# Performance work log

Hardware: AMD Instinct MI355X
Metric: run time of the kernel (lower is better)

## Reference

```python
import jax, jax.numpy as jnp
import numpy as np

B, L, V = 16, 2048, 64


def setup_inputs() -> dict:
    key = jax.random.key(0)
    k1, k2, k3, k4 = jax.random.split(key, 4)
    idx = jax.random.randint(k1, (B, L), 0, V)                      # tokens
    Wq_w = jax.random.normal(k2, (V, V), jnp.float32) * 0.02         # nn.Linear weight
    Wv_w = jax.random.normal(k3, (V, V), jnp.float32) * 0.02 + np.float32(np.e)  # Wv.weight (+e init)
    v_emb = jax.random.normal(k4, (L, 1), jnp.float32) * 0.02        # nn.Embedding(length, 1)
    return {"idx": idx, "Wq_w": Wq_w, "Wv_w": Wv_w, "v_emb": v_emb}


def reference(idx, Wq_w, Wv_w, v_emb):
    Lx = v_emb.shape[0]
    Vx = Wq_w.shape[0]
    # e = one_hot token embedding, [B, L, V]
    e = jax.nn.one_hot(idx, Vx, dtype=jnp.float32)
    i = jnp.arange(Lx)
    # pos[i, j] = max(i - j, 0); learned relative-position score table [L, L]
    pos = jnp.maximum(i[:, None] - i[None, :], 0)
    pos_embd = v_emb[pos, 0]
    causal = i[:, None] >= i[None, :]                                # tril mask
    # Attention block 1: scores are the learned position table (no QK^T)
    attn1 = jax.nn.softmax(jnp.where(causal, pos_embd, -jnp.inf), axis=-1)  # [L, L]
    l1 = jnp.einsum('ts,bsv->btv', attn1, e)                         # [B, L, V]
    # Attention block 2: Wq(e) @ l1^T, masked softmax, attn @ e * scalar
    q = jnp.einsum('btv,uv->btu', e, Wq_w)                           # F.linear: e @ Wq^T
    scores = jnp.einsum('btv,bsv->bts', q, l1)                       # [B, L, L]
    attn2 = jax.nn.softmax(jnp.where(causal, scores, -jnp.inf), axis=-1)
    l2 = jnp.einsum('bts,bsv->btv', attn2, e) * Wv_w[0, 0]           # logits [B, L, V]
    return l2
```

## Files before the change

### kernel.cpp

```cpp
#include <hip/hip_runtime.h>


#define LSEQ 2048
#define NB 16
#define NV 64
#define NC 32

typedef __attribute__((ext_vector_type(8))) short bf16x8;
typedef __attribute__((ext_vector_type(4))) float f32x4;

__device__ __forceinline__ unsigned short f2bf(float f) {
  unsigned int u = __float_as_uint(f);
  return (unsigned short)((u + 0x7FFFu + ((u >> 16) & 1u)) >> 16);
}

__global__ __launch_bounds__(256) void k_gather(const int* __restrict__ idx,
                                                const float* __restrict__ Wq,
                                                const float* __restrict__ v_emb,
                                                unsigned short* __restrict__ Agr,
                                                unsigned short* __restrict__ Ebf,
                                                float* __restrict__ S) {
  const int b = blockIdx.x >> 4;
  const int tile = blockIdx.x & 15;
  const int w = threadIdx.x >> 6;
  const int lane = threadIdx.x & 63;

  if (blockIdx.x == 0 && threadIdx.x < 64) {
    const int base = lane * 32;
    float e[32];
    float run = 0.f;
#pragma unroll
    for (int i = 0; i < 32; ++i) { e[i] = expf(v_emb[base + i]); run += e[i]; }
    float incl = run;
#pragma unroll
    for (int d = 1; d < 64; d <<= 1) {
      float up = __shfl_up(incl, d);
      if (lane >= d) incl += up;
    }
    float acc = incl - run;
#pragma unroll
    for (int i = 0; i < 32; ++i) {
      acc += e[i];
      Ebf[base + i] = f2bf(e[i]);
      S[base + i] = acc;
    }
  }

  const int k8base = tile * 16 + w * 4;
#pragma unroll
  for (int r = 0; r < 4; ++r) {
    const int k8 = k8base + r;
    unsigned short v[8];
#pragma unroll
    for (int j = 0; j < 8; ++j) {
      const int ii = idx[b * LSEQ + (2047 - (k8 * 8 + j))];
      v[j] = f2bf(Wq[ii * 64 + lane]);
    }
    uint4 st;
    st.x = (unsigned int)v[0] | ((unsigned int)v[1] << 16);
    st.y = (unsigned int)v[2] | ((unsigned int)v[3] << 16);
    st.z = (unsigned int)v[4] | ((unsigned int)v[5] << 16);
    st.w = (unsigned int)v[6] | ((unsigned int)v[7] << 16);
    *(uint4*)(Agr + ((size_t)(b * 256 + k8) * 64 + lane) * 8) = st;
  }
}

__global__ __launch_bounds__(256) void k_gemm(const unsigned short* __restrict__ Agr,
                                              const unsigned short* __restrict__ Ebf,
                                              const float* __restrict__ S,
                                              float* __restrict__ P) {
  __shared__ unsigned short GL0[2208];
  __shared__ unsigned short GL1[2176];
  __shared__ float red[16][64];
  __shared__ float red2[16][64];

  const int b  = blockIdx.y;
  const int bn = 63 - (int)blockIdx.x;
  const int n0 = bn * 32;
  const int tid = threadIdx.x;
  const int w = tid >> 6;
  const int lane = tid & 63;
  const int quad = lane >> 4;
  const int lm = lane & 15;
  const int nsub = w & 1;
  const int kh = w >> 1;

  {
    const int wend = n0 + 160;
    for (int i = 96 + tid; i < wend; i += 256) {
      const int e0 = i - 127;
      const int e1 = i - 126;
      GL0[i] = (e0 >= 0 && e0 < LSEQ) ? Ebf[e0] : (unsigned short)0;
      GL1[i] = (e1 >= 0 && e1 < LSEQ) ? Ebf[e1] : (unsigned short)0;
    }
  }
  __syncthreads();

  f32x4 acc[4];
#pragma unroll
  for (int mt = 0; mt < 4; ++mt) acc[mt] = (f32x4){0.f, 0.f, 0.f, 0.f};

  const int nbase = n0 + nsub * 16;
  const int sbase = nbase + lm - 1920;
  const int kstart = 2048 - (n0 + 32);
  const int iters = bn + 1;
  const unsigned short* __restrict__ abase = Agr + (size_t)b * 256 * 64 * 8;

  union AF { uint4 u; bf16x8 v; };
  union BF { unsigned int u[4]; bf16x8 v; };
  AF a[3][4];
  BF bb[3];

#define LOAD_FRAGS(J_, SL) do {                                             \
    const int k_ = kstart + (kh + 2 * (J_)) * 32;                           \
    const int kq8_ = (k_ >> 3) + quad;                                      \
    const unsigned short* ab_ = abase + ((size_t)kq8_ * 64 + lm) * 8;       \
    a[SL][0].u = *(const uint4*)(ab_ + 0 * 128);                            \
    a[SL][1].u = *(const uint4*)(ab_ + 1 * 128);                            \
    a[SL][2].u = *(const uint4*)(ab_ + 2 * 128);                            \
    a[SL][3].u = *(const uint4*)(ab_ + 3 * 128);                            \
    const int s_ = sbase + k_ + quad * 8;                                   \
    const unsigned int* gb_ = (s_ & 1) ? (const unsigned int*)GL1           \
                                       : (const unsigned int*)GL0;          \
    const int off_ = s_ >> 1;                                               \
    bb[SL].u[0] = gb_[off_ + 0]; bb[SL].u[1] = gb_[off_ + 1];               \
    bb[SL].u[2] = gb_[off_ + 2]; bb[SL].u[3] = gb_[off_ + 3];               \
  } while (0)

#define MFMA4(SL) do {                                                      \
    acc[0] = __builtin_amdgcn_mfma_f32_16x16x32_bf16(a[SL][0].v, bb[SL].v, acc[0], 0, 0, 0); \
    acc[1] = __builtin_amdgcn_mfma_f32_16x16x32_bf16(a[SL][1].v, bb[SL].v, acc[1], 0, 0, 0); \
    acc[2] = __builtin_amdgcn_mfma_f32_16x16x32_bf16(a[SL][2].v, bb[SL].v, acc[2], 0, 0, 0); \
    acc[3] = __builtin_amdgcn_mfma_f32_16x16x32_bf16(a[SL][3].v, bb[SL].v, acc[3], 0, 0, 0); \
  } while (0)

  const int J = (iters > kh) ? ((iters - kh + 1) >> 1) : 0;
  if (J > 0) {
    LOAD_FRAGS(0, 0);
    if (J > 1) LOAD_FRAGS(1, 1);
    int j = 0;
    while (true) {
      if (j + 2 < J) LOAD_FRAGS(j + 2, 2);
      MFMA4(0);
      if (++j >= J) break;
      if (j + 2 < J) LOAD_FRAGS(j + 2, 0);
      MFMA4(1);
      if (++j >= J) break;
      if (j + 2 < J) LOAD_FRAGS(j + 2, 1);
      MFMA4(2);
      if (++j >= J) break;
    }
  }
#undef LOAD_FRAGS
#undef MFMA4

  if (kh == 1) {
    float (*rd)[64] = nsub ? red2 : red;
#pragma unroll
    for (int mt = 0; mt < 4; ++mt)
#pragma unroll
      for (int r = 0; r < 4; ++r) rd[mt * 4 + r][lane] = acc[mt][r];
  }
  __syncthreads();
  if (kh == 0) {
    float (*rd)[64] = nsub ? red2 : red;
#pragma unroll
    for (int mt = 0; mt < 4; ++mt)
#pragma unroll
      for (int r = 0; r < 4; ++r) acc[mt][r] += rd[mt * 4 + r][lane];

    const float sinv = 1.0f / S[nbase + lm];
#pragma unroll
    for (int mt = 0; mt < 4; ++mt) {
#pragma unroll
      for (int r = 0; r < 4; ++r) {
        const int c = mt * 16 + quad * 4 + r;
        P[((size_t)(b * 64 + c)) * LSEQ + nbase + lm] = __expf(acc[mt][r] * sinv);
      }
    }
  }
}

__global__ __launch_bounds__(256) void k_scanemit(const int* __restrict__ idx,
                                                  const float* __restrict__ P,
                                                  const float* __restrict__ Wv,
                                                  float* __restrict__ out) {
  __shared__ float Hs[NC][65];
  __shared__ float bins[4][64];
  const int bc = blockIdx.x;
  const int b = bc >> 6;
  const int c = bc & 63;
  const int w = threadIdx.x >> 6;
  const int lane = threadIdx.x & 63;

  const float* __restrict__ prow = P + (size_t)bc * LSEQ;
  const int* __restrict__ irow = idx + b * LSEQ;

  float p[8]; int ii[8];
#pragma unroll
  for (int r = 0; r < 8; ++r) {
    const int ch = w * 8 + r;
    p[r] = prow[ch * 64 + lane];
    ii[r] = irow[ch * 64 + lane];
  }
  for (int i = threadIdx.x; i < NC * 65; i += 256) ((float*)Hs)[i] = 0.f;
  __syncthreads();
#pragma unroll
  for (int r = 0; r < 8; ++r) atomicAdd(&Hs[w * 8 + r][ii[r]], p[r]);
  __syncthreads();

  const int half = lane >> 5, l32 = lane & 31;
#pragma unroll
  for (int r = 0; r < 8; ++r) {
    const int v = w * 16 + r * 2 + half;
    const float h = Hs[l32][v];
    float x = h;
#pragma unroll
    for (int d = 1; d < 32; d <<= 1) {
      float up = __shfl_up(x, d, 32);
      if (l32 >= d) x += up;
    }
    Hs[l32][v] = x - h;
  }
  __syncthreads();

  const float wv = Wv[0];
#pragma unroll
  for (int r = 0; r < 8; ++r) {
    const int ch = w * 8 + r;
    unsigned long long m = __ballot(ii[r] == c);
    while (m) {
      const int srel = __builtin_ctzll(m);
      m &= m - 1;
      const int t = ch * 64 + srel;
      const float pm = (lane <= srel) ? p[r] : 0.f;
      bins[w][lane] = 0.f;
      __threadfence_block();
      atomicAdd(&bins[w][ii[r]], pm);
      __threadfence_block();
      const float bin = bins[w][lane] + Hs[ch][lane];
      float z = bin;
#pragma unroll
      for (int d = 1; d < 64; d <<= 1) z += __shfl_xor(z, d);
      out[((size_t)(b * LSEQ + t)) * 64 + lane] = wv * bin / z;
    }
  }
}

extern "C" void kernel_launch(void* const* d_in, const int* in_sizes, int n_in,
                              void* d_out, int out_size, void* d_ws, size_t ws_size,
                              hipStream_t stream) {
  const int* idx     = (const int*)d_in[0];
  const float* Wq    = (const float*)d_in[1];
  const float* Wv    = (const float*)d_in[2];
  const float* v_emb = (const float*)d_in[3];
  float* out = (float*)d_out;

  float* S = (float*)d_ws;
  float* P = S + LSEQ;
  unsigned short* Ebf = (unsigned short*)(P + (size_t)NB * NV * LSEQ);
  unsigned short* Agr = Ebf + LSEQ;

  k_gather<<<NB * 16, 256, 0, stream>>>(idx, Wq, v_emb, Agr, Ebf, S);
  k_gemm<<<dim3(64, NB), 256, 0, stream>>>(Agr, Ebf, S, P);
  k_scanemit<<<NB * NV, 256, 0, stream>>>(idx, P, Wv, out);
}
```

Measured before the change: 120.6 us.

## Fuse gather, GEMM and scan-emit into one cooperative kernel with grid syncs

Replaces three separate kernel launches with one cooperative persistent kernel of 512 blocks that runs the gather, GEMM and scan/emit phases separated by grid-wide syncs. The GEMM phase pairs causal column tiles (bn and 63-bn) per block to balance the triangular work, and stages the position-table rows in shared memory. The aim is to remove inter-kernel launch gaps and tail effects. In exchange it adds grid-sync cost and fixes the phase shapes to the cooperative grid size. If the cooperative launch fails, it falls back to the original three kernels.

New measurement: 259.1 us. 115% more time.

```diff
diff --git a/kernel.cpp b/kernel.cpp
--- a/kernel.cpp
+++ b/kernel.cpp
@@ -1,4 +1,7 @@
 #include <hip/hip_runtime.h>
+#include <hip/hip_cooperative_groups.h>
+
+namespace cg = cooperative_groups;
 
 
 #define LSEQ 2048
@@ -12,6 +15,247 @@
 __device__ __forceinline__ unsigned short f2bf(float f) {
   unsigned int u = __float_as_uint(f);
   return (unsigned short)((u + 0x7FFFu + ((u >> 16) & 1u)) >> 16);
+}
+
+__global__ __launch_bounds__(256, 2) void k_fused(
+    const int* __restrict__ idx, const float* __restrict__ Wq,
+    const float* __restrict__ Wv, const float* __restrict__ v_emb,
+    unsigned short* __restrict__ Agr, unsigned short* __restrict__ Ebf,
+    float* __restrict__ S, float* __restrict__ P, float* __restrict__ out) {
+  union SMem {
+    struct {
+      unsigned short GL0[2208];
+      unsigned short GL1[2176];
+      float red[16][64];
+      float red2[16][64];
+    } g;
+    struct {
+      float Hs[NC][65];
+      float bins[4][64];
+    } s;
+  };
+  __shared__ SMem sm;
+
+  const int bid = blockIdx.x;
+  const int tid = threadIdx.x;
+  const int w = tid >> 6;
+  const int lane = tid & 63;
+
+  {
+    const int b = bid >> 5;
+    const int sub = bid & 31;
+
+    if (bid == 0 && tid < 64) {
+      const int base = lane * 32;
+      float e[32];
+      float run = 0.f;
+#pragma unroll
+      for (int i = 0; i < 32; ++i) { e[i] = expf(v_emb[base + i]); run += e[i]; }
+      float incl = run;
+#pragma unroll
+      for (int d = 1; d < 64; d <<= 1) {
+        float up = __shfl_up(incl, d);
+        if (lane >= d) incl += up;
+      }
+      float acc = incl - run;
+#pragma unroll
+      for (int i = 0; i < 32; ++i) {
+        acc += e[i];
+        Ebf[base + i] = f2bf(e[i]);
+        S[base + i] = acc;
+      }
+    }
+
+    const int k8base = sub * 8 + w * 2;
+#pragma unroll
+    for (int r = 0; r < 2; ++r) {
+      const int k8 = k8base + r;
+      unsigned short v[8];
+#pragma unroll
+      for (int j = 0; j < 8; ++j) {
+        const int ii = idx[b * LSEQ + (2047 - (k8 * 8 + j))];
+        v[j] = f2bf(Wq[ii * 64 + lane]);
+      }
+      uint4 st;
+      st.x = (unsigned int)v[0] | ((unsigned int)v[1] << 16);
+      st.y = (unsigned int)v[2] | ((unsigned int)v[3] << 16);
+      st.z = (unsigned int)v[4] | ((unsigned int)v[5] << 16);
+      st.w = (unsigned int)v[6] | ((unsigned int)v[7] << 16);
+      *(uint4*)(Agr + ((size_t)(b * 256 + k8) * 64 + lane) * 8) = st;
+    }
+  }
+  cg::this_grid().sync();
+
+  {
+    const int b = bid >> 5;
+    const int jj = bid & 31;
+    const int quad = lane >> 4;
+    const int lm = lane & 15;
+    const int nsub = w & 1;
+    const int kh = w >> 1;
+    const unsigned short* __restrict__ abase = Agr + (size_t)b * 256 * 64 * 8;
+
+    {
+      const int wend = (63 - jj) * 32 + 160;
+      for (int i = 96 + tid; i < wend; i += 256) {
+        const int e0 = i - 127;
+        const int e1 = i - 126;
+        sm.g.GL0[i] = (e0 >= 0 && e0 < LSEQ) ? Ebf[e0] : (unsigned short)0;
+        sm.g.GL1[i] = (e1 >= 0 && e1 < LSEQ) ? Ebf[e1] : (unsigned short)0;
+      }
+    }
+    __syncthreads();
+
+    for (int half = 0; half < 2; ++half) {
+      const int bn = half ? jj : (63 - jj);
+      const int n0 = bn * 32;
+      const int nbase = n0 + nsub * 16;
+      const int sbase = nbase + lm - 1920;
+      const int kstart = 2048 - (n0 + 32);
+      const int iters = bn + 1;
+
+      f32x4 acc[4];
+#pragma unroll
+      for (int mt = 0; mt < 4; ++mt) acc[mt] = (f32x4){0.f, 0.f, 0.f, 0.f};
+
+      union AF { uint4 u; bf16x8 v; };
+      union BF { unsigned int u[4]; bf16x8 v; };
+      AF a[3][4];
+      BF bb[3];
+
+#define LOAD_FRAGS(J_, SL) do {                                             \
+    const int k_ = kstart + (kh + 2 * (J_)) * 32;                           \
+    const int kq8_ = (k_ >> 3) + quad;                                      \
+    const unsigned short* ab_ = abase + ((size_t)kq8_ * 64 + lm) * 8;       \
+    a[SL][0].u = *(const uint4*)(ab_ + 0 * 128);                            \
+    a[SL][1].u = *(const uint4*)(ab_ + 1 * 128);                            \
+    a[SL][2].u = *(const uint4*)(ab_ + 2 * 128);                            \
+    a[SL][3].u = *(const uint4*)(ab_ + 3 * 128);                            \
+    const int s_ = sbase + k_ + quad * 8;                                   \
+    const unsigned int* gb_ = (s_ & 1) ? (const unsigned int*)sm.g.GL1      \
+                                       : (const unsigned int*)sm.g.GL0;     \
+    const int off_ = s_ >> 1;                                               \
+    bb[SL].u[0] = gb_[off_ + 0]; bb[SL].u[1] = gb_[off_ + 1];               \
+    bb[SL].u[2] = gb_[off_ + 2]; bb[SL].u[3] = gb_[off_ + 3];               \
+  } while (0)
+
+#define MFMA4(SL) do {                                                      \
+    acc[0] = __builtin_amdgcn_mfma_f32_16x16x32_bf16(a[SL][0].v, bb[SL].v, acc[0], 0, 0, 0); \
+    acc[1] = __builtin_amdgcn_mfma_f32_16x16x32_bf16(a[SL][1].v, bb[SL].v, acc[1], 0, 0, 0); \
+    acc[2] = __builtin_amdgcn_mfma_f32_16x16x32_bf16(a[SL][2].v, bb[SL].v, acc[2], 0, 0, 0); \
+    acc[3] = __builtin_amdgcn_mfma_f32_16x16x32_bf16(a[SL][3].v, bb[SL].v, acc[3], 0, 0, 0); \
+  } while (0)
+
+      const int J = (iters > kh) ? ((iters - kh + 1) >> 1) : 0;
+      if (J > 0) {
+        LOAD_FRAGS(0, 0);
+        if (J > 1) LOAD_FRAGS(1, 1);
+        int j = 0;
+        while (true) {
+          if (j + 2 < J) LOAD_FRAGS(j + 2, 2);
+          MFMA4(0);
+          if (++j >= J) break;
+          if (j + 2 < J) LOAD_FRAGS(j + 2, 0);
+          MFMA4(1);
+          if (++j >= J) break;
+          if (j + 2 < J) LOAD_FRAGS(j + 2, 1);
+          MFMA4(2);
+          if (++j >= J) break;
+        }
+      }
+#undef LOAD_FRAGS
+#undef MFMA4
+
+      if (kh == 1) {
+        float (*rd)[64] = nsub ? sm.g.red2 : sm.g.red;
+#pragma unroll
+        for (int mt = 0; mt < 4; ++mt)
+#pragma unroll
+          for (int r = 0; r < 4; ++r) rd[mt * 4 + r][lane] = acc[mt][r];
+      }
+      __syncthreads();
+      if (kh == 0) {
+        float (*rd)[64] = nsub ? sm.g.red2 : sm.g.red;
+#pragma unroll
+        for (int mt = 0; mt < 4; ++mt)
+#pragma unroll
+          for (int r = 0; r < 4; ++r) acc[mt][r] += rd[mt * 4 + r][lane];
+
+        const float sinv = 1.0f / S[nbase + lm];
+#pragma unroll
+        for (int mt = 0; mt < 4; ++mt) {
+#pragma unroll
+          for (int r = 0; r < 4; ++r) {
+            const int c = mt * 16 + quad * 4 + r;
+            P[((size_t)(b * 64 + c)) * LSEQ + nbase + lm] = __expf(acc[mt][r] * sinv);
+          }
+        }
+      }
+      __syncthreads();
+    }
+  }
+  cg::this_grid().sync();
+
+  {
+    for (int q = 0; q < 2; ++q) {
+      const int bc = (bid << 1) | q;
+      const int b2 = bc >> 6;
+      const int c = bc & 63;
+      const float* __restrict__ prow = P + (size_t)bc * LSEQ;
+      const int* __restrict__ irow = idx + b2 * LSEQ;
+
+      float p[8]; int ii[8];
+#pragma unroll
+      for (int r = 0; r < 8; ++r) {
+        const int ch = w * 8 + r;
+        p[r] = prow[ch * 64 + lane];
+        ii[r] = irow[ch * 64 + lane];
+      }
+      __syncthreads();
+      for (int i = tid; i < NC * 65; i += 256) ((float*)sm.s.Hs)[i] = 0.f;
+      __syncthreads();
+#pragma unroll
+      for (int r = 0; r < 8; ++r) atomicAdd(&sm.s.Hs[w * 8 + r][ii[r]], p[r]);
+      __syncthreads();
+
+      const int hhalf = lane >> 5, l32 = lane & 31;
+#pragma unroll
+      for (int r = 0; r < 8; ++r) {
+        const int v = w * 16 + r * 2 + hhalf;
+        const float h = sm.s.Hs[l32][v];
+        float x = h;
+#pragma unroll
+        for (int d = 1; d < 32; d <<= 1) {
+          float up = __shfl_up(x, d, 32);
+          if (l32 >= d) x += up;
+        }
+        sm.s.Hs[l32][v] = x - h;
+      }
+      __syncthreads();
+
+      const float wv = Wv[0];
+#pragma unroll
+      for (int r = 0; r < 8; ++r) {
+        const int ch = w * 8 + r;
+        unsigned long long m = __ballot(ii[r] == c);
+        while (m) {
+          const int srel = __builtin_ctzll(m);
+          m &= m - 1;
+          const int t = ch * 64 + srel;
+          const float pm = (lane <= srel) ? p[r] : 0.f;
+          sm.s.bins[w][lane] = 0.f;
+          __threadfence_block();
+          atomicAdd(&sm.s.bins[w][ii[r]], pm);
+          __threadfence_block();
+          const float bin = sm.s.bins[w][lane] + sm.s.Hs[ch][lane];
+          float z = bin;
+#pragma unroll
+          for (int d = 1; d < 64; d <<= 1) z += __shfl_xor(z, d);
+          out[((size_t)(b2 * LSEQ + t)) * 64 + lane] = wv * bin / z;
+        }
+      }
+    }
+  }
 }
 
 __global__ __launch_bounds__(256) void k_gather(const int* __restrict__ idx,
@@ -261,7 +505,20 @@
   unsigned short* Ebf = (unsigned short*)(P + (size_t)NB * NV * LSEQ);
   unsigned short* Agr = Ebf + LSEQ;
 
-  k_gather<<<NB * 16, 256, 0, stream>>>(idx, Wq, v_emb, Agr, Ebf, S);
-  k_gemm<<<dim3(64, NB), 256, 0, stream>>>(Agr, Ebf, S, P);
-  k_scanemit<<<NB * NV, 256, 0, stream>>>(idx, P, Wv, out);
+  const int* a_idx = idx; const float* a_Wq = Wq; const float* a_Wv = Wv;
+  const float* a_vemb = v_emb;
+  unsigned short* a_Agr = Agr; unsigned short* a_Ebf = Ebf;
+  float* a_S = S; float* a_P = P; float* a_out = out;
+  void* args[] = {(void*)&a_idx, (void*)&a_Wq, (void*)&a_Wv, (void*)&a_vemb,
+                  (void*)&a_Agr, (void*)&a_Ebf, (void*)&a_S, (void*)&a_P,
+                  (void*)&a_out};
+
+  hipError_t cerr = hipLaunchCooperativeKernel((void*)k_fused, dim3(512),
+                                               dim3(256), args, 0, stream);
+  if (cerr != hipSuccess) {
+    (void)hipGetLastError();
+    k_gather<<<NB * 16, 256, 0, stream>>>(idx, Wq, v_emb, Agr, Ebf, S);
+    k_gemm<<<dim3(64, NB), 256, 0, stream>>>(Agr, Ebf, S, P);
+    k_scanemit<<<NB * NV, 256, 0, stream>>>(idx, P, Wv, out);
+  }
 }
```
